# Kernel tuning notes

Hardware: AMD Instinct MI355X
Metric: run time of the kernel (lower is better)

## Reference

```python
import math
import jax, jax.numpy as jnp
import numpy as np

D_MODEL = 1024
N_HEADS = 16
HEAD_DIM = D_MODEL // N_HEADS
B, S = 4, 1024


def setup_inputs() -> dict:
    key = jax.random.key(0)
    ks = jax.random.split(key, 20)
    def lin(kw, kb):
        # torch nn.Linear: weight [out, in], y = x @ W.T + b
        w = jax.random.normal(kw, (D_MODEL, D_MODEL), jnp.float32) * 0.02
        b = jax.random.normal(kb, (D_MODEL,), jnp.float32) * 0.02
        return w, b
    inp = {
        'global_feat': jax.random.normal(ks[0], (B, S, D_MODEL), jnp.float32),
        'local_feat': jax.random.normal(ks[1], (B, S, D_MODEL), jnp.float32),
        'text_feat': jax.random.normal(ks[2], (B, S, D_MODEL), jnp.float32),
    }
    names = ['glb_q', 'glb_k', 'glb_v', 'plb_q', 'plb_k', 'plb_v', 'dense']
    for i, n in enumerate(names):
        w, b = lin(ks[3 + 2 * i], ks[4 + 2 * i])
        inp[n + '_w'] = w
        inp[n + '_b'] = b
    return inp


def _heads(x):
    # [B,S,D] -> [B,H,S,dh]
    b, s, _ = x.shape
    return x.reshape(b, s, N_HEADS, HEAD_DIM).transpose(0, 2, 1, 3)


def _merge(x):
    # [B,H,S,dh] -> [B,S,D]
    b, h, s, d = x.shape
    return x.transpose(0, 2, 1, 3).reshape(b, s, h * d)


def reference(global_feat, local_feat, text_feat,
              glb_q_w, glb_q_b, glb_k_w, glb_k_b, glb_v_w, glb_v_b,
              plb_q_w, plb_q_b, plb_k_w, plb_k_b, plb_v_w, plb_v_b,
              dense_w, dense_b):
    scale = 1.0 / math.sqrt(HEAD_DIM)
    gq = _heads(global_feat @ glb_q_w.T + glb_q_b)
    gk = _heads(local_feat @ glb_k_w.T + glb_k_b)
    gv = _heads(local_feat @ glb_v_w.T + glb_v_b)
    pq = _heads(local_feat @ plb_q_w.T + plb_q_b)
    pk = _heads(text_feat @ plb_k_w.T + plb_k_b)
    pv = _heads(text_feat @ plb_v_w.T + plb_v_b)

    glb_probs = jax.nn.softmax(jnp.einsum('bhqd,bhkd->bhqk', gq, gk) * scale, axis=-1)
    plb_probs = jax.nn.softmax(jnp.einsum('bhqd,bhkd->bhqk', pq, pk) * scale, axis=-1)

    # bridge: matmul of the two probability matrices (dropout disabled / eval)
    plb_enhanced = jnp.einsum('bhql,bhlt->bhqt', glb_probs, plb_probs)

    glb_ctx = jnp.einsum('bhqk,bhkd->bhqd', glb_probs, gv)
    plb_ctx = jnp.einsum('bhqt,bhtd->bhqd', plb_enhanced, pv)

    last = _merge(glb_ctx) + _merge(plb_ctx)
    return last @ dense_w.T + dense_b
```

## Files before the change

kernel.cpp:

```cpp
#include <hip/hip_runtime.h>


#define DEVI static __device__ __forceinline__

typedef __attribute__((ext_vector_type(4))) float f32x4;
typedef __attribute__((ext_vector_type(8))) __bf16 bf16x8;
typedef __attribute__((ext_vector_type(8))) short s16x8;
typedef __attribute__((ext_vector_type(4))) short s16x4;

constexpr int S = 1024, D = 1024, NH = 16, DH = 64, NB = 4;
constexpr int M = NB * S;
constexpr int KD = 1024;
constexpr int ND = 1024;
constexpr float QSCALE = 0.18033688011112042f;

DEVI short f2bf(float f) {
  unsigned u = __builtin_bit_cast(unsigned, f);
  u += 0x7FFFu + ((u >> 16) & 1u);
  return (short)(u >> 16);
}

DEVI f32x4 mfma_bf16(s16x8 a, s16x8 b, f32x4 c) {
  return __builtin_amdgcn_mfma_f32_16x16x32_bf16(
      __builtin_bit_cast(bf16x8, a), __builtin_bit_cast(bf16x8, b), c, 0, 0, 0);
}

DEVI void gll16(const void* g, void* l) {
  __builtin_amdgcn_global_load_lds(
      (const __attribute__((address_space(1))) unsigned*)g,
      (__attribute__((address_space(3))) unsigned*)l, 16, 0, 0);
}

struct Ptrs3 { const float* p0; const float* p1; const float* p2; };
struct Ptrs7 { const float* p[7]; };

__global__ __launch_bounds__(256) void cast_inputs(Ptrs3 in, short* __restrict__ out) {
  int b = blockIdx.x;
  int which = b >> 12;
  const float* src = which == 0 ? in.p0 : (which == 1 ? in.p1 : in.p2);
  size_t local = ((size_t)(b & 4095) * 256 + threadIdx.x) * 4;
  f32x4 v = *(const f32x4*)(src + local);
  s16x4 o = { f2bf(v[0]), f2bf(v[1]), f2bf(v[2]), f2bf(v[3]) };
  *(s16x4*)(out + (size_t)which * ((size_t)M * KD) + local) = o;
}

__global__ __launch_bounds__(256) void cast_weights(Ptrs7 in, short* __restrict__ out) {
  int b = blockIdx.x;
  int which = b >> 10;
  size_t local = ((size_t)(b & 1023) * 256 + threadIdx.x) * 4;
  f32x4 v = *(const f32x4*)(in.p[which] + local);
  s16x4 o = { f2bf(v[0]), f2bf(v[1]), f2bf(v[2]), f2bf(v[3]) };
  *(s16x4*)(out + (size_t)which * 1048576 + local) = o;
}

struct GemmBatch {
  const short* A[6];
  const float* bias[6];
  void* out[6];
};

__global__ __launch_bounds__(256) void gemm_proj(GemmBatch gb, const short* __restrict__ W) {
  __shared__ short As[128 * 32];
  __shared__ short Bs[128 * 32];
  const int z = blockIdx.z;
  const short* A = gb.A[z];
  const short* Bw = W + (size_t)z * ((size_t)KD * ND);
  const float* bias = gb.bias[z];
  const float scale = (z == 0 || z == 3) ? QSCALE : 1.0f;
  const int f32out = (z == 2);

  const int tid = threadIdx.x;
  const int lane = tid & 63, wave = tid >> 6;
  const int wr = wave >> 1, wc = wave & 1;
  const int l15 = lane & 15, lg = lane >> 4;
  const int rowBase = blockIdx.y * 128, colBase = blockIdx.x * 128;

  const int cr = tid >> 2, co = (tid & 3) * 8;
  const short* gA0 = A + (size_t)(rowBase + cr) * KD + co;
  const short* gA1 = A + (size_t)(rowBase + 64 + cr) * KD + co;
  const short* gB0 = Bw + (size_t)(colBase + cr) * KD + co;
  const short* gB1 = Bw + (size_t)(colBase + 64 + cr) * KD + co;
  short* lA0 = As + tid * 8;
  short* lA1 = As + (tid + 256) * 8;
  short* lB0 = Bs + tid * 8;
  short* lB1 = Bs + (tid + 256) * 8;

  f32x4 acc[4][4] = {};
  for (int k0 = 0; k0 < KD; k0 += 32) {
    __syncthreads();
    gll16(gA0 + k0, lA0);
    gll16(gA1 + k0, lA1);
    gll16(gB0 + k0, lB0);
    gll16(gB1 + k0, lB1);
    __syncthreads();
    s16x8 af[4], bf[4];
#pragma unroll
    for (int m = 0; m < 4; m++)
      af[m] = *(const s16x8*)(As + (wr * 64 + m * 16 + l15) * 32 + lg * 8);
#pragma unroll
    for (int n = 0; n < 4; n++)
      bf[n] = *(const s16x8*)(Bs + (wc * 64 + n * 16 + l15) * 32 + lg * 8);
#pragma unroll
    for (int m = 0; m < 4; m++)
#pragma unroll
      for (int n = 0; n < 4; n++)
        acc[m][n] = mfma_bf16(af[m], bf[n], acc[m][n]);
  }

  const int r0 = lg * 4;
#pragma unroll
  for (int m = 0; m < 4; m++)
#pragma unroll
    for (int n = 0; n < 4; n++)
#pragma unroll
      for (int i = 0; i < 4; i++) {
        int row = rowBase + wr * 64 + m * 16 + r0 + i;
        int col = colBase + wc * 64 + n * 16 + l15;
        float v = (acc[m][n][i] + bias[col]) * scale;
        size_t idx = (((size_t)(row >> 10) * NH + (col >> 6)) * S + (row & (S - 1))) * DH + (col & (DH - 1));
        if (f32out) ((float*)gb.out[z])[idx] = v;
        else        ((short*)gb.out[z])[idx] = f2bf(v);
      }
}

__global__ __launch_bounds__(256) void gemm_dense(const short* __restrict__ A,
                                                  const short* __restrict__ Bw,
                                                  const float* __restrict__ bias,
                                                  float* __restrict__ outp) {
  __shared__ short As[128 * 32];
  __shared__ short Bs[128 * 32];
  const int tid = threadIdx.x;
  const int lane = tid & 63, wave = tid >> 6;
  const int wr = wave >> 1, wc = wave & 1;
  const int l15 = lane & 15, lg = lane >> 4;
  const int rowBase = blockIdx.y * 128, colBase = blockIdx.x * 128;

  const int cr = tid >> 2, co = (tid & 3) * 8;
  const short* gA0 = A + (size_t)(rowBase + cr) * KD + co;
  const short* gA1 = A + (size_t)(rowBase + 64 + cr) * KD + co;
  const short* gB0 = Bw + (size_t)(colBase + cr) * KD + co;
  const short* gB1 = Bw + (size_t)(colBase + 64 + cr) * KD + co;
  short* lA0 = As + tid * 8;
  short* lA1 = As + (tid + 256) * 8;
  short* lB0 = Bs + tid * 8;
  short* lB1 = Bs + (tid + 256) * 8;

  f32x4 acc[4][4] = {};
  for (int k0 = 0; k0 < KD; k0 += 32) {
    __syncthreads();
    gll16(gA0 + k0, lA0);
    gll16(gA1 + k0, lA1);
    gll16(gB0 + k0, lB0);
    gll16(gB1 + k0, lB1);
    __syncthreads();
    s16x8 af[4], bf[4];
#pragma unroll
    for (int m = 0; m < 4; m++)
      af[m] = *(const s16x8*)(As + (wr * 64 + m * 16 + l15) * 32 + lg * 8);
#pragma unroll
    for (int n = 0; n < 4; n++)
      bf[n] = *(const s16x8*)(Bs + (wc * 64 + n * 16 + l15) * 32 + lg * 8);
#pragma unroll
    for (int m = 0; m < 4; m++)
#pragma unroll
      for (int n = 0; n < 4; n++)
        acc[m][n] = mfma_bf16(af[m], bf[n], acc[m][n]);
  }

  const int r0 = lg * 4;
#pragma unroll
  for (int m = 0; m < 4; m++)
#pragma unroll
    for (int n = 0; n < 4; n++)
#pragma unroll
      for (int i = 0; i < 4; i++) {
        int row = rowBase + wr * 64 + m * 16 + r0 + i;
        int col = colBase + wc * 64 + n * 16 + l15;
        outp[(size_t)row * ND + col] = acc[m][n][i] + bias[col];
      }
}

__global__ __launch_bounds__(256) void transpose_bf16(const short* __restrict__ in,
                                                      short* __restrict__ out) {
  __shared__ short t[64 * 65];
  const int bh = blockIdx.y, s0 = blockIdx.x * 64;
  const int tid = threadIdx.x;
#pragma unroll
  for (int j = 0; j < 16; j++) {
    int e = j * 256 + tid;
    int s = e >> 6, d = e & 63;
    t[d * 65 + s] = in[((size_t)bh * S + s0 + s) * DH + d];
  }
  __syncthreads();
#pragma unroll
  for (int j = 0; j < 16; j++) {
    int e = j * 256 + tid;
    int d = e >> 6, s = e & 63;
    out[((size_t)bh * DH + d) * S + s0 + s] = t[d * 65 + s];
  }
}

__global__ __launch_bounds__(256) void vprime_t(const float* __restrict__ gv,
                                                const float* __restrict__ pa,
                                                short* __restrict__ out) {
  __shared__ short t[64 * 65];
  const int bh = blockIdx.y, s0 = blockIdx.x * 64;
  const int tid = threadIdx.x;
#pragma unroll
  for (int j = 0; j < 16; j++) {
    int e = j * 256 + tid;
    int s = e >> 6, d = e & 63;
    size_t idx = ((size_t)bh * S + s0 + s) * DH + d;
    t[d * 65 + s] = f2bf(gv[idx] + pa[idx]);
  }
  __syncthreads();
#pragma unroll
  for (int j = 0; j < 16; j++) {
    int e = j * 256 + tid;
    int d = e >> 6, s = e & 63;
    out[((size_t)bh * DH + d) * S + s0 + s] = t[d * 65 + s];
  }
}

DEVI void stage_kv(const short* kb, const short* vb, int kt,
                   short* KT, short* VTs, int tid) {
  const int r0 = tid >> 3, cb = (tid & 7) * 16;
  const int r1 = r0 + 32;
  const int sw0 = (r0 & 7) << 4;
  gll16((const char*)kb + (size_t)(kt + r0) * 128 + (cb ^ sw0), KT + tid * 8);
  gll16((const char*)kb + (size_t)(kt + r1) * 128 + (cb ^ sw0), KT + (tid + 256) * 8);
  gll16((const char*)vb + (size_t)r0 * 2048 + (size_t)kt * 2 + (cb ^ sw0), VTs + tid * 8);
  gll16((const char*)vb + (size_t)r1 * 2048 + (size_t)kt * 2 + (cb ^ sw0), VTs + (tid + 256) * 8);
}

template <int OUTMODE>
__global__ __launch_bounds__(256, 4) void attn64(const short* __restrict__ Q,
                                                 const short* __restrict__ Km,
                                                 const short* __restrict__ Vt,
                                                 void* __restrict__ outp) {
  __shared__ short KT[2][64 * 64];
  __shared__ short VTs[2][64 * 64];
  __shared__ short Pl[4][1024];
  const int tid = threadIdx.x, lane = tid & 63, wave = tid >> 6;
  const int l15 = lane & 15, lg = lane >> 4;
  const int w = blockIdx.x;
  const int sw = (w & 7) * 128 + (w >> 3);
  const int bh = sw >> 4;
  const int q0 = (sw & 15) * 64 + wave * 16;

  const short* qp = Q + ((size_t)bh * S + q0 + l15) * DH + lg * 8;
  s16x8 qf0 = *(const s16x8*)qp;
  s16x8 qf1 = *(const s16x8*)(qp + 32);

  const short* kb = Km + (size_t)bh * S * DH;
  const short* vb = Vt + (size_t)bh * DH * S;
  short* myP = Pl[wave];
  const int rsz = (l15 & 7) << 3;

  stage_kv(kb, vb, 0, KT[0], VTs[0], tid);
  __syncthreads();

  f32x4 acc[4] = {};
  float lrow[4] = {0.f, 0.f, 0.f, 0.f};

  for (int kt = 0; kt < S; kt += 64) {
    const int cur = (kt >> 6) & 1;
    if (kt + 64 < S) stage_kv(kb, vb, kt + 64, KT[cur ^ 1], VTs[cur ^ 1], tid);

    f32x4 sf[4];
#pragma unroll
    for (int n = 0; n < 4; n++) {
      const short* kr = KT[cur] + (n * 16 + l15) * 64;
      s16x8 k0 = *(const s16x8*)(kr + ((lg * 8) ^ rsz));
      s16x8 k1 = *(const s16x8*)(kr + ((32 + lg * 8) ^ rsz));
      sf[n] = mfma_bf16(qf0, k0, f32x4{});
      sf[n] = mfma_bf16(qf1, k1, sf[n]);
    }

    f32x4 p[4];
    float ts[4];
#pragma unroll
    for (int n = 0; n < 4; n++)
#pragma unroll
      for (int i = 0; i < 4; i++) p[n][i] = exp2f(sf[n][i]);
#pragma unroll
    for (int i = 0; i < 4; i++) ts[i] = (p[0][i] + p[1][i]) + (p[2][i] + p[3][i]);
#pragma unroll
    for (int off = 1; off < 16; off <<= 1)
#pragma unroll
      for (int i = 0; i < 4; i++) ts[i] += __shfl_xor(ts[i], off);
#pragma unroll
    for (int i = 0; i < 4; i++) lrow[i] += ts[i];

#pragma unroll
    for (int n = 0; n < 4; n++)
#pragma unroll
      for (int i = 0; i < 4; i++) {
        int row = lg * 4 + i;
        myP[row * 64 + ((n * 16 + l15) ^ ((row & 7) << 3))] = f2bf(p[n][i]);
      }
    asm volatile("s_waitcnt lgkmcnt(0)" ::: "memory");
    s16x8 pa0 = *(const s16x8*)(myP + l15 * 64 + ((lg * 8) ^ rsz));
    s16x8 pa1 = *(const s16x8*)(myP + l15 * 64 + ((32 + lg * 8) ^ rsz));

#pragma unroll
    for (int n = 0; n < 4; n++) {
      const short* vr = VTs[cur] + (n * 16 + l15) * 64;
      s16x8 v0 = *(const s16x8*)(vr + ((lg * 8) ^ rsz));
      s16x8 v1 = *(const s16x8*)(vr + ((32 + lg * 8) ^ rsz));
      acc[n] = mfma_bf16(pa0, v0, acc[n]);
      acc[n] = mfma_bf16(pa1, v1, acc[n]);
    }

    __syncthreads();
  }

  float inv[4];
#pragma unroll
  for (int i = 0; i < 4; i++) inv[i] = 1.f / lrow[i];
#pragma unroll
  for (int n = 0; n < 4; n++)
#pragma unroll
    for (int i = 0; i < 4; i++) {
      int qq = q0 + lg * 4 + i;
      int dc = n * 16 + l15;
      float v = acc[n][i] * inv[i];
      if (OUTMODE == 0)
        ((float*)outp)[((size_t)bh * S + qq) * DH + dc] = v;
      else
        ((short*)outp)[((size_t)(bh >> 4) * S + qq) * D + (bh & 15) * DH + dc] = f2bf(v);
    }
}

extern "C" void kernel_launch(void* const* d_in, const int* in_sizes, int n_in,
                              void* d_out, int out_size, void* d_ws, size_t ws_size,
                              hipStream_t stream) {
  const float* xg = (const float*)d_in[0];
  const float* xl = (const float*)d_in[1];
  const float* xt = (const float*)d_in[2];
  const float* wf[7]; const float* bf_[7];
  for (int i = 0; i < 7; i++) { wf[i] = (const float*)d_in[3 + 2 * i]; bf_[i] = (const float*)d_in[4 + 2 * i]; }

  char* ws = (char*)d_ws;
  size_t off = 0;
  auto alloc = [&](size_t bytes) { void* p = ws + off; off += (bytes + 255) & ~(size_t)255; return p; };
  short* x16   = (short*)alloc((size_t)3 * M * KD * 2);
  short* w16   = (short*)alloc((size_t)7 * KD * ND * 2);
  short* gq16  = (short*)alloc((size_t)M * D * 2);
  short* gk16  = (short*)alloc((size_t)M * D * 2);
  float* gv32  = (float*)alloc((size_t)M * D * 4);
  short* pq16  = (short*)alloc((size_t)M * D * 2);
  short* pk16  = (short*)alloc((size_t)M * D * 2);
  short* pv16  = (short*)alloc((size_t)M * D * 2);
  short* pvt16 = (short*)alloc((size_t)M * D * 2);
  float* plb32 = (float*)alloc((size_t)M * D * 4);
  short* vpt16 = (short*)alloc((size_t)M * D * 2);
  short* last16= (short*)alloc((size_t)M * D * 2);
  (void)ws_size; (void)in_sizes; (void)n_in; (void)out_size;

  short* xg16 = x16;
  short* xl16 = x16 + (size_t)M * KD;
  short* xt16 = x16 + (size_t)2 * M * KD;

  Ptrs3 p3{xg, xl, xt};
  cast_inputs<<<3 * 4096, 256, 0, stream>>>(p3, x16);
  Ptrs7 p7; for (int i = 0; i < 7; i++) p7.p[i] = wf[i];
  cast_weights<<<7 * 1024, 256, 0, stream>>>(p7, w16);

  GemmBatch gb;
  gb.A[0] = xg16; gb.A[1] = xl16; gb.A[2] = xl16; gb.A[3] = xl16; gb.A[4] = xt16; gb.A[5] = xt16;
  for (int i = 0; i < 6; i++) gb.bias[i] = bf_[i];
  gb.out[0] = gq16; gb.out[1] = gk16; gb.out[2] = gv32;
  gb.out[3] = pq16; gb.out[4] = pk16; gb.out[5] = pv16;
  dim3 gg(ND / 128, M / 128, 6);
  gemm_proj<<<gg, 256, 0, stream>>>(gb, w16);

  dim3 gt(S / 64, NB * NH);
  transpose_bf16<<<gt, 256, 0, stream>>>(pv16, pvt16);
  attn64<0><<<1024, 256, 0, stream>>>(pq16, pk16, pvt16, plb32);
  vprime_t<<<gt, 256, 0, stream>>>(gv32, plb32, vpt16);
  attn64<1><<<1024, 256, 0, stream>>>(gq16, gk16, vpt16, last16);

  dim3 gd(ND / 128, M / 128);
  gemm_dense<<<gd, 256, 0, stream>>>(last16, w16 + (size_t)6 * 1048576, bf_[6], (float*)d_out);
}
```

Before: 357.9 us.

## Double-buffer GEMM LDS with swizzle, remap blocks, compute softmax row sums via MFMA

```diff
diff --git a/kernel.cpp b/kernel.cpp
--- a/kernel.cpp
+++ b/kernel.cpp
@@ -53,6 +53,17 @@
   *(s16x4*)(out + (size_t)which * 1048576 + local) = o;
 }
 
+DEVI void stage_ab(const short* A, const short* Bw, int rowBase, int colBase, int k0,
+                   short* Asb, short* Bsb, int tid) {
+  const int cr = tid >> 2;
+  const int cb = (tid & 3) * 16;
+  const int sw = ((cr >> 1) & 3) << 4;
+  gll16((const char*)(A + (size_t)(rowBase + cr) * KD + k0) + (cb ^ sw), Asb + tid * 8);
+  gll16((const char*)(A + (size_t)(rowBase + 64 + cr) * KD + k0) + (cb ^ sw), Asb + (tid + 256) * 8);
+  gll16((const char*)(Bw + (size_t)(colBase + cr) * KD + k0) + (cb ^ sw), Bsb + tid * 8);
+  gll16((const char*)(Bw + (size_t)(colBase + 64 + cr) * KD + k0) + (cb ^ sw), Bsb + (tid + 256) * 8);
+}
+
 struct GemmBatch {
   const short* A[6];
   const float* bias[6];
@@ -60,9 +71,13 @@
 };
 
 __global__ __launch_bounds__(256) void gemm_proj(GemmBatch gb, const short* __restrict__ W) {
-  __shared__ short As[128 * 32];
-  __shared__ short Bs[128 * 32];
-  const int z = blockIdx.z;
+  __shared__ short As[2][128 * 32];
+  __shared__ short Bs[2][128 * 32];
+  const int wg = (blockIdx.x & 7) * 192 + (blockIdx.x >> 3);
+  const int z = wg >> 8;
+  const int rem = wg & 255;
+  const int rowBase = (rem >> 3) * 128, colBase = (rem & 7) * 128;
+
   const short* A = gb.A[z];
   const short* Bw = W + (size_t)z * ((size_t)KD * ND);
   const float* bias = gb.bias[z];
@@ -73,38 +88,30 @@
   const int lane = tid & 63, wave = tid >> 6;
   const int wr = wave >> 1, wc = wave & 1;
   const int l15 = lane & 15, lg = lane >> 4;
-  const int rowBase = blockIdx.y * 128, colBase = blockIdx.x * 128;
-
-  const int cr = tid >> 2, co = (tid & 3) * 8;
-  const short* gA0 = A + (size_t)(rowBase + cr) * KD + co;
-  const short* gA1 = A + (size_t)(rowBase + 64 + cr) * KD + co;
-  const short* gB0 = Bw + (size_t)(colBase + cr) * KD + co;
-  const short* gB1 = Bw + (size_t)(colBase + 64 + cr) * KD + co;
-  short* lA0 = As + tid * 8;
-  short* lA1 = As + (tid + 256) * 8;
-  short* lB0 = Bs + tid * 8;
-  short* lB1 = Bs + (tid + 256) * 8;
+  const int rs = ((l15 >> 1) & 3) << 3;
+
+  stage_ab(A, Bw, rowBase, colBase, 0, As[0], Bs[0], tid);
+  __syncthreads();
 
   f32x4 acc[4][4] = {};
+  int buf = 0;
   for (int k0 = 0; k0 < KD; k0 += 32) {
-    __syncthreads();
-    gll16(gA0 + k0, lA0);
-    gll16(gA1 + k0, lA1);
-    gll16(gB0 + k0, lB0);
-    gll16(gB1 + k0, lB1);
-    __syncthreads();
+    if (k0 + 32 < KD)
+      stage_ab(A, Bw, rowBase, colBase, k0 + 32, As[buf ^ 1], Bs[buf ^ 1], tid);
     s16x8 af[4], bf[4];
 #pragma unroll
     for (int m = 0; m < 4; m++)
-      af[m] = *(const s16x8*)(As + (wr * 64 + m * 16 + l15) * 32 + lg * 8);
-#pragma unroll
-    for (int n = 0; n < 4; n++)
-      bf[n] = *(const s16x8*)(Bs + (wc * 64 + n * 16 + l15) * 32 + lg * 8);
+      af[m] = *(const s16x8*)(As[buf] + (wr * 64 + m * 16 + l15) * 32 + ((lg * 8) ^ rs));
+#pragma unroll
+    for (int n = 0; n < 4; n++)
+      bf[n] = *(const s16x8*)(Bs[buf] + (wc * 64 + n * 16 + l15) * 32 + ((lg * 8) ^ rs));
 #pragma unroll
     for (int m = 0; m < 4; m++)
 #pragma unroll
       for (int n = 0; n < 4; n++)
         acc[m][n] = mfma_bf16(af[m], bf[n], acc[m][n]);
+    __syncthreads();
+    buf ^= 1;
   }
 
   const int r0 = lg * 4;
@@ -127,44 +134,39 @@
                                                   const short* __restrict__ Bw,
                                                   const float* __restrict__ bias,
                                                   float* __restrict__ outp) {
-  __shared__ short As[128 * 32];
-  __shared__ short Bs[128 * 32];
+  __shared__ short As[2][128 * 32];
+  __shared__ short Bs[2][128 * 32];
+  const int wg = (blockIdx.x & 7) * 32 + (blockIdx.x >> 3);
+  const int rowBase = (wg >> 3) * 128, colBase = (wg & 7) * 128;
+
   const int tid = threadIdx.x;
   const int lane = tid & 63, wave = tid >> 6;
   const int wr = wave >> 1, wc = wave & 1;
   const int l15 = lane & 15, lg = lane >> 4;
-  const int rowBase = blockIdx.y * 128, colBase = blockIdx.x * 128;
-
-  const int cr = tid >> 2, co = (tid & 3) * 8;
-  const short* gA0 = A + (size_t)(rowBase + cr) * KD + co;
-  const short* gA1 = A + (size_t)(rowBase + 64 + cr) * KD + co;
-  const short* gB0 = Bw + (size_t)(colBase + cr) * KD + co;
-  const short* gB1 = Bw + (size_t)(colBase + 64 + cr) * KD + co;
-  short* lA0 = As + tid * 8;
-  short* lA1 = As + (tid + 256) * 8;
-  short* lB0 = Bs + tid * 8;
-  short* lB1 = Bs + (tid + 256) * 8;
+  const int rs = ((l15 >> 1) & 3) << 3;
+
+  stage_ab(A, Bw, rowBase, colBase, 0, As[0], Bs[0], tid);
+  __syncthreads();
 
   f32x4 acc[4][4] = {};
+  int buf = 0;
   for (int k0 = 0; k0 < KD; k0 += 32) {
-    __syncthreads();
-    gll16(gA0 + k0, lA0);
-    gll16(gA1 + k0, lA1);
-    gll16(gB0 + k0, lB0);
-    gll16(gB1 + k0, lB1);
-    __syncthreads();
+    if (k0 + 32 < KD)
+      stage_ab(A, Bw, rowBase, colBase, k0 + 32, As[buf ^ 1], Bs[buf ^ 1], tid);
     s16x8 af[4], bf[4];
 #pragma unroll
     for (int m = 0; m < 4; m++)
-      af[m] = *(const s16x8*)(As + (wr * 64 + m * 16 + l15) * 32 + lg * 8);
-#pragma unroll
-    for (int n = 0; n < 4; n++)
-      bf[n] = *(const s16x8*)(Bs + (wc * 64 + n * 16 + l15) * 32 + lg * 8);
+      af[m] = *(const s16x8*)(As[buf] + (wr * 64 + m * 16 + l15) * 32 + ((lg * 8) ^ rs));
+#pragma unroll
+    for (int n = 0; n < 4; n++)
+      bf[n] = *(const s16x8*)(Bs[buf] + (wc * 64 + n * 16 + l15) * 32 + ((lg * 8) ^ rs));
 #pragma unroll
     for (int m = 0; m < 4; m++)
 #pragma unroll
       for (int n = 0; n < 4; n++)
         acc[m][n] = mfma_bf16(af[m], bf[n], acc[m][n]);
+    __syncthreads();
+    buf ^= 1;
   }
 
   const int r0 = lg * 4;
@@ -256,12 +258,13 @@
   const short* vb = Vt + (size_t)bh * DH * S;
   short* myP = Pl[wave];
   const int rsz = (l15 & 7) << 3;
+  const s16x8 ones = { 0x3F80, 0x3F80, 0x3F80, 0x3F80, 0x3F80, 0x3F80, 0x3F80, 0x3F80 };
 
   stage_kv(kb, vb, 0, KT[0], VTs[0], tid);
   __syncthreads();
 
   f32x4 acc[4] = {};
-  float lrow[4] = {0.f, 0.f, 0.f, 0.f};
+  f32x4 accS = {};
 
   for (int kt = 0; kt < S; kt += 64) {
     const int cur = (kt >> 6) & 1;
@@ -278,19 +281,10 @@
     }
 
     f32x4 p[4];
-    float ts[4];
 #pragma unroll
     for (int n = 0; n < 4; n++)
 #pragma unroll
       for (int i = 0; i < 4; i++) p[n][i] = exp2f(sf[n][i]);
-#pragma unroll
-    for (int i = 0; i < 4; i++) ts[i] = (p[0][i] + p[1][i]) + (p[2][i] + p[3][i]);
-#pragma unroll
-    for (int off = 1; off < 16; off <<= 1)
-#pragma unroll
-      for (int i = 0; i < 4; i++) ts[i] += __shfl_xor(ts[i], off);
-#pragma unroll
-    for (int i = 0; i < 4; i++) lrow[i] += ts[i];
 
 #pragma unroll
     for (int n = 0; n < 4; n++)
@@ -303,6 +297,9 @@
     s16x8 pa0 = *(const s16x8*)(myP + l15 * 64 + ((lg * 8) ^ rsz));
     s16x8 pa1 = *(const s16x8*)(myP + l15 * 64 + ((32 + lg * 8) ^ rsz));
 
+    accS = mfma_bf16(pa0, ones, accS);
+    accS = mfma_bf16(pa1, ones, accS);
+
 #pragma unroll
     for (int n = 0; n < 4; n++) {
       const short* vr = VTs[cur] + (n * 16 + l15) * 64;
@@ -317,7 +314,7 @@
 
   float inv[4];
 #pragma unroll
-  for (int i = 0; i < 4; i++) inv[i] = 1.f / lrow[i];
+  for (int i = 0; i < 4; i++) inv[i] = 1.f / accS[i];
 #pragma unroll
   for (int n = 0; n < 4; n++)
 #pragma unroll
@@ -372,8 +369,7 @@
   for (int i = 0; i < 6; i++) gb.bias[i] = bf_[i];
   gb.out[0] = gq16; gb.out[1] = gk16; gb.out[2] = gv32;
   gb.out[3] = pq16; gb.out[4] = pk16; gb.out[5] = pv16;
-  dim3 gg(ND / 128, M / 128, 6);
-  gemm_proj<<<gg, 256, 0, stream>>>(gb, w16);
+  gemm_proj<<<1536, 256, 0, stream>>>(gb, w16);
 
   dim3 gt(S / 64, NB * NH);
   transpose_bf16<<<gt, 256, 0, stream>>>(pv16, pvt16);
@@ -381,6 +377,5 @@
   vprime_t<<<gt, 256, 0, stream>>>(gv32, plb32, vpt16);
   attn64<1><<<1024, 256, 0, stream>>>(gq16, gk16, vpt16, last16);
 
-  dim3 gd(ND / 128, M / 128);
-  gemm_dense<<<gd, 256, 0, stream>>>(last16, w16 + (size_t)6 * 1048576, bf_[6], (float*)d_out);
-}
+  gemm_dense<<<256, 256, 0, stream>>>(last16, w16 + (size_t)6 * 1048576, bf_[6], (float*)d_out);
+}
```

Result: faster. 326.1 us (-8.9%).
